# Kernel tuning notes

Measured on AMD Instinct MI355X. Metric: run time of the kernel, lower is better.

Reference implementation:

```python
import jax, jax.numpy as jnp
import numpy as np

LOG_2PI = np.float32(np.log(2.0 * np.pi))


def _expect(features, labels, pi, mu, sigma):
    # features [N,A], labels [N], pi [C,K], mu [C,K,A], sigma [C,K,A,A]
    d = features.shape[1]
    K = pi.shape[1]
    pi_n = pi[labels]                      # [N,K]
    mu_n = mu[labels]                      # [N,K,A]
    # invert / slogdet per (class, cluster) once, then gather (same math as
    # inverting the per-sample gathered sigma, but C*K inversions not N*K)
    inv_sigma = jnp.linalg.inv(sigma)[labels]          # [N,K,A,A]
    logdet = jnp.linalg.slogdet(sigma)[1][labels]      # [N,K]
    diff = features[:, None, :] - mu_n                 # [N,K,A]
    dist = jnp.einsum('nkd,nkde,nke->nk', diff, inv_sigma, diff)
    # NOTE: sign of the d*log(2pi) term follows the original code verbatim
    log_p = -(dist - d * LOG_2PI + logdet) / 2.0       # [N,K]
    onehot = jax.nn.one_hot(jnp.argmax(log_p, axis=1), K, dtype=features.dtype)
    q_un = onehot * pi_n
    return q_un / (q_un.sum(axis=1, keepdims=True) + 1e-30)


def setup_inputs() -> dict:
    key = jax.random.key(0)
    ks = jax.random.split(key, 6)
    N, C, K, A = 2048, 100, 4, 128
    features = jax.random.normal(ks[0], (N, A), dtype=jnp.float32)
    weight = jax.random.normal(ks[1], (C, A), dtype=jnp.float32) * 0.05
    bias = jnp.zeros((C,), dtype=jnp.float32)
    pi = jax.random.uniform(ks[2], (C, K), dtype=jnp.float32) + 0.1
    pi = pi / pi.sum(axis=1, keepdims=True)
    mu = jax.random.normal(ks[3], (C, K, A), dtype=jnp.float32)
    # SPD covariance stack: B B^T / A + I
    B = jax.random.normal(ks[4], (C, K, A, A), dtype=jnp.float32) * 0.3
    sigma = jnp.einsum('ckij,cklj->ckil', B, B) / A + jnp.eye(A, dtype=jnp.float32)
    labels = jax.random.randint(ks[5], (N,), 0, C, dtype=jnp.int64)
    ratio = jnp.float32(0.5)
    return {"features": features, "weight": weight, "bias": bias,
            "pi": pi, "mu": mu, "sigma": sigma, "labels": labels,
            "ratio": ratio}


def reference(features, weight, bias, pi, mu, sigma, labels, ratio):
    N, A = features.shape
    C, K = pi.shape
    y = features @ weight.T + bias                     # fc(features)  [N,C]
    # NxW_ij - NxW_kj : row j of W minus row label[n] of W, per sample
    diff_w = weight[None, :, :] - weight[labels][:, None, :]   # [N,C,A]
    q = _expect(features, labels, pi, mu, sigma)               # [N,K]
    onehot_q = jax.nn.one_hot(jnp.argmax(q, axis=1), K, dtype=features.dtype)
    CV = jnp.einsum('nkde,nk->nde', sigma[labels], onehot_q)   # [N,A,A]
    # diagonal of ratio * (dW) CV (dW)^T, computed without the [N,C,C] matrix
    sigma2 = ratio * jnp.einsum('nca,nab,ncb->nc', diff_w, CV, diff_w)
    aug = y + 0.5 * sigma2                                     # [N,C]
    logp = jax.nn.log_softmax(aug, axis=-1)
    loss = -jnp.mean(jnp.take_along_axis(logp, labels[:, None], axis=1))
    return (loss, y)
```

## Files before the change

kernel.cpp:

```cpp
#include <hip/hip_runtime.h>
#include <hip/hip_bf16.h>
#include <cmath>

#define N_S    2048
#define C_CLS  100
#define K_CL   4
#define A_DIM  128
#define LDSROW 132
#define NB     16
#define MAXPER 96
#define WTPAD  101
#define SPB    8

__global__ __launch_bounds__(256) void k_bucket(
    const int* __restrict__ labels, int* __restrict__ cntg, int* __restrict__ idxg)
{
    __shared__ int cntL[C_CLS];
    const int t = threadIdx.x;
    if (t < C_CLS) cntL[t] = 0;
    __syncthreads();
    for (int n = t; n < N_S; n += 256) {
        int c = labels[n];
        int slot = atomicAdd(&cntL[c], 1);
        if (slot < MAXPER) idxg[c * MAXPER + slot] = n;
    }
    __syncthreads();
    if (t < C_CLS) cntg[t] = min(cntL[t], MAXPER);
}

__device__ __forceinline__ float gj_invert_lds(
    float* As, float* Rbuf, float* DinvS, int tid)
{
    const int lane = tid & 63;
    const int wv   = tid >> 6;
    float logdet = 0.0f;

    for (int t = 0; t < 8; ++t) {
        const int p0 = NB * t;

        if (wv == 0) {
            const int r = lane >> 2, cg = lane & 3;
            float4 dv = *(const float4*)&As[(p0 + r) * LDSROW + p0 + 4 * cg];
            #pragma unroll
            for (int p = 0; p < NB; ++p) {
                const int sel = p & 3, pr4 = p >> 2;
                float te = (sel == 0) ? dv.x : (sel == 1) ? dv.y : (sel == 2) ? dv.z : dv.w;
                float piv = __shfl(te, (p << 2) | pr4, 64);
                float ip  = 1.0f / piv;
                logdet += __logf(piv);
                const int rowsrc = (p << 2) | cg;
                float4 prs;
                prs.x = __shfl(dv.x, rowsrc, 64) * ip;
                prs.y = __shfl(dv.y, rowsrc, 64) * ip;
                prs.z = __shfl(dv.z, rowsrc, 64) * ip;
                prs.w = __shfl(dv.w, rowsrc, 64) * ip;
                if (cg == pr4) (&prs.x)[sel] = ip;
                float f = __shfl(te, (lane & ~3) | pr4, 64);
                if (r == p) {
                    dv = prs;
                } else {
                    dv.x -= f * prs.x; dv.y -= f * prs.y;
                    dv.z -= f * prs.z; dv.w -= f * prs.w;
                    if (cg == pr4) (&dv.x)[sel] = -f * ip;
                }
            }
            DinvS[r * 17 + 4 * cg + 0] = dv.x;
            DinvS[r * 17 + 4 * cg + 1] = dv.y;
            DinvS[r * 17 + 4 * cg + 2] = dv.z;
            DinvS[r * 17 + 4 * cg + 3] = dv.w;
        }
        __syncthreads();

        {
            const int rr = tid >> 5, j4c = tid & 31;
            float4 o;
            if ((j4c >> 2) == t) {
                const int cg = j4c & 3;
                o.x = DinvS[rr * 17 + 4 * cg + 0];
                o.y = DinvS[rr * 17 + 4 * cg + 1];
                o.z = DinvS[rr * 17 + 4 * cg + 2];
                o.w = DinvS[rr * 17 + 4 * cg + 3];
            } else {
                o.x = 0.f; o.y = 0.f; o.z = 0.f; o.w = 0.f;
                #pragma unroll 4
                for (int k = 0; k < NB; ++k) {
                    const float a = DinvS[rr * 17 + k];
                    const float4 s4 = *(const float4*)&As[(p0 + k) * LDSROW + 4 * j4c];
                    o.x += a * s4.x; o.y += a * s4.y; o.z += a * s4.z; o.w += a * s4.w;
                }
            }
            *(float4*)&Rbuf[rr * A_DIM + 4 * j4c] = o;
        }
        __syncthreads();

        if (tid < 448) {
            const int rgi = tid >> 4;
            const int cp  = tid & 15;
            const int rga = (rgi < 4 * t) ? rgi : rgi + 4;
            const int row0 = 4 * rga;
            const int c0 = 8 * cp, c1 = 8 * cp + 4;
            const bool pcol = ((cp >> 1) == t);
            float4 a00, a01, a10, a11, a20, a21, a30, a31;
            if (pcol) {
                a00 = a01 = a10 = a11 = a20 = a21 = a30 = a31 = (float4){0, 0, 0, 0};
            } else {
                a00 = *(const float4*)&As[(row0 + 0) * LDSROW + c0];
                a01 = *(const float4*)&As[(row0 + 0) * LDSROW + c1];
                a10 = *(const float4*)&As[(row0 + 1) * LDSROW + c0];
                a11 = *(const float4*)&As[(row0 + 1) * LDSROW + c1];
                a20 = *(const float4*)&As[(row0 + 2) * LDSROW + c0];
                a21 = *(const float4*)&As[(row0 + 2) * LDSROW + c1];
                a30 = *(const float4*)&As[(row0 + 3) * LDSROW + c0];
                a31 = *(const float4*)&As[(row0 + 3) * LDSROW + c1];
            }
            #pragma unroll 4
            for (int k = 0; k < NB; ++k) {
                const float4 r0 = *(const float4*)&Rbuf[k * A_DIM + c0];
                const float4 r1 = *(const float4*)&Rbuf[k * A_DIM + c1];
                const float f0 = As[(row0 + 0) * LDSROW + p0 + k];
                const float f1 = As[(row0 + 1) * LDSROW + p0 + k];
                const float f2 = As[(row0 + 2) * LDSROW + p0 + k];
                const float f3 = As[(row0 + 3) * LDSROW + p0 + k];
                a00.x -= f0 * r0.x; a00.y -= f0 * r0.y; a00.z -= f0 * r0.z; a00.w -= f0 * r0.w;
                a01.x -= f0 * r1.x; a01.y -= f0 * r1.y; a01.z -= f0 * r1.z; a01.w -= f0 * r1.w;
                a10.x -= f1 * r0.x; a10.y -= f1 * r0.y; a10.z -= f1 * r0.z; a10.w -= f1 * r0.w;
                a11.x -= f1 * r1.x; a11.y -= f1 * r1.y; a11.z -= f1 * r1.z; a11.w -= f1 * r1.w;
                a20.x -= f2 * r0.x; a20.y -= f2 * r0.y; a20.z -= f2 * r0.z; a20.w -= f2 * r0.w;
                a21.x -= f2 * r1.x; a21.y -= f2 * r1.y; a21.z -= f2 * r1.z; a21.w -= f2 * r1.w;
                a30.x -= f3 * r0.x; a30.y -= f3 * r0.y; a30.z -= f3 * r0.z; a30.w -= f3 * r0.w;
                a31.x -= f3 * r1.x; a31.y -= f3 * r1.y; a31.z -= f3 * r1.z; a31.w -= f3 * r1.w;
            }
            *(float4*)&As[(row0 + 0) * LDSROW + c0] = a00;
            *(float4*)&As[(row0 + 0) * LDSROW + c1] = a01;
            *(float4*)&As[(row0 + 1) * LDSROW + c0] = a10;
            *(float4*)&As[(row0 + 1) * LDSROW + c1] = a11;
            *(float4*)&As[(row0 + 2) * LDSROW + c0] = a20;
            *(float4*)&As[(row0 + 2) * LDSROW + c1] = a21;
            *(float4*)&As[(row0 + 3) * LDSROW + c0] = a30;
            *(float4*)&As[(row0 + 3) * LDSROW + c1] = a31;
        }
        {
            const int rr = tid >> 5, j4c = tid & 31;
            *(float4*)&As[(p0 + rr) * LDSROW + 4 * j4c] =
                *(const float4*)&Rbuf[rr * A_DIM + 4 * j4c];
        }
        __syncthreads();
    }
    return logdet;
}

__global__ __launch_bounds__(512, 2) void k_invert_score(
    const float* __restrict__ sigma, const float* __restrict__ mu,
    const float* __restrict__ features, const int* __restrict__ cntg,
    const int* __restrict__ idxg, float* __restrict__ score)
{
    __shared__ __align__(16) float As[A_DIM * LDSROW];
    __shared__ __align__(16) float Scratch[NB * A_DIM + 16*33];
    __shared__ float DinvS[NB * 17];
    __shared__ float ldS;

    const int tid = threadIdx.x;
    const int bid = blockIdx.x;
    const int cl  = bid >> 2;

    const float4* src = (const float4*)(sigma + (size_t)bid * A_DIM * A_DIM);
    for (int e4 = tid; e4 < A_DIM * 32; e4 += 512) {
        int i = e4 >> 5, j4 = e4 & 31;
        *(float4*)&As[i * LDSROW + 4 * j4] = src[e4];
    }
    __syncthreads();

    float logdet = gj_invert_lds(As, Scratch, DinvS, tid);
    if (tid == 0) ldS = logdet;
    __syncthreads();
    const float ld = ldS;

    float* Dbuf = Scratch;
    float* Par  = Scratch + NB * A_DIM;
    const int s16 = tid >> 5;
    const int fc  = tid & 31;
    const int cnt = cntg[cl];
    const float4 muv = ((const float4*)mu)[bid * 32 + fc];

    for (int c0 = 0; c0 < cnt; c0 += 16) {
        const int m = cnt - c0 < 16 ? cnt - c0 : 16;
        if (s16 < m) {
            const int n = idxg[cl * MAXPER + c0 + s16];
            const float4 f = ((const float4*)features)[n * 32 + fc];
            float4 dv;
            dv.x = f.x - muv.x; dv.y = f.y - muv.y;
            dv.z = f.z - muv.z; dv.w = f.w - muv.w;
            *(float4*)&Dbuf[s16 * A_DIM + 4 * fc] = dv;
        }
        __syncthreads();
        if (s16 < m) {
            float4 p = {0.f, 0.f, 0.f, 0.f};
            #pragma unroll 4
            for (int i = 0; i < A_DIM; ++i) {
                const float  d = Dbuf[s16 * A_DIM + i];
                const float4 a = *(const float4*)&As[i * LDSROW + 4 * fc];
                p.x += d * a.x; p.y += d * a.y; p.z += d * a.z; p.w += d * a.w;
            }
            const float4 dj = *(const float4*)&Dbuf[s16 * A_DIM + 4 * fc];
            Par[s16 * 33 + fc] = p.x * dj.x + p.y * dj.y + p.z * dj.z + p.w * dj.w;
        }
        __syncthreads();
        if (tid < m) {
            const int n = idxg[cl * MAXPER + c0 + tid];
            float q = 0.f;
            #pragma unroll
            for (int j = 0; j < 32; ++j) q += Par[tid * 33 + j];
            score[n * K_CL + (bid & 3)] = q + ld;
        }
        __syncthreads();
    }
}

template<int R>
__device__ __forceinline__ void gsweep(
    const float* __restrict__ Ss, const float* __restrict__ weight,
    int c0, int lane, float wc0, float wc1, int bid,
    float* __restrict__ gdiag, float* __restrict__ gcol)
{
    const int c0u = __builtin_amdgcn_readfirstlane(c0);
    const float* __restrict__ wr = weight + (size_t)c0u * A_DIM;
    float h0[R], h1[R];
    #pragma unroll
    for (int r = 0; r < R; ++r) { h0[r] = 0.f; h1[r] = 0.f; }
    #pragma unroll 2
    for (int i = 0; i < A_DIM; ++i) {
        const float s0 = Ss[i * A_DIM + lane];
        const float s1 = Ss[i * A_DIM + 64 + lane];
        #pragma unroll
        for (int r = 0; r < R; ++r) {
            const float b = wr[r * A_DIM + i];
            h0[r] += b * s0; h1[r] += b * s1;
        }
    }
    #pragma unroll
    for (int r = 0; r < R; ++r) {
        const int c = c0 + r;
        float pd = h0[r] * weight[c * A_DIM + lane]
                 + h1[r] * weight[c * A_DIM + 64 + lane];
        float pc = h0[r] * wc0 + h1[r] * wc1;
        #pragma unroll
        for (int off = 32; off; off >>= 1) {
            pd += __shfl_xor(pd, off, 64);
            pc += __shfl_xor(pc, off, 64);
        }
        if (lane == 0) {
            gdiag[bid * C_CLS + c] = pd;
            gcol [bid * C_CLS + c] = pc;
        }
    }
}

__global__ __launch_bounds__(256, 2) void k_gprep(
    const float* __restrict__ sigma, const float* __restrict__ weight,
    float* __restrict__ gdiag, float* __restrict__ gcol)
{
    __shared__ __align__(16) float Ss[A_DIM * A_DIM];
    const int tid = threadIdx.x, bid = blockIdx.x;
    const int cl  = bid >> 2;
    const int lane = tid & 63, wv = tid >> 6;

    const float4* src = (const float4*)(sigma + (size_t)bid * A_DIM * A_DIM);
    for (int e4 = tid; e4 < A_DIM * 32; e4 += 256)
        ((float4*)Ss)[e4] = src[e4];
    __syncthreads();

    const float wc0 = weight[cl * A_DIM + lane];
    const float wc1 = weight[cl * A_DIM + 64 + lane];
    const int cbeg = wv * 25;

    gsweep<10>(Ss, weight, cbeg,      lane, wc0, wc1, bid, gdiag, gcol);
    gsweep<10>(Ss, weight, cbeg + 10, lane, wc0, wc1, bid, gdiag, gcol);
    gsweep<5> (Ss, weight, cbeg + 20, lane, wc0, wc1, bid, gdiag, gcol);
}

__global__ __launch_bounds__(256) void k_out(
    const float* __restrict__ features, const float* __restrict__ weight,
    const float* __restrict__ bias, const int* __restrict__ labels,
    const float* __restrict__ score, const float* __restrict__ gdiag,
    const float* __restrict__ gcol, const float* __restrict__ ratio_p,
    float* __restrict__ y, float* __restrict__ loss)
{
    __shared__ float Wt[A_DIM * WTPAD];
    __shared__ float bs[C_CLS];
    __shared__ __align__(16) float xs[2][A_DIM];
    __shared__ float red[2][2], red2[2][2], acl_s[2], lsum;

    const int tid  = threadIdx.x;
    const int half = tid >> 7;
    const int t    = tid & 127;

    for (int u = tid; u < C_CLS * 32; u += 256) {
        const int c = u >> 5, j4 = u & 31;
        const float4 w = ((const float4*)weight)[u];
        Wt[(4 * j4 + 0) * WTPAD + c] = w.x;
        Wt[(4 * j4 + 1) * WTPAD + c] = w.y;
        Wt[(4 * j4 + 2) * WTPAD + c] = w.z;
        Wt[(4 * j4 + 3) * WTPAD + c] = w.w;
    }
    if (tid < C_CLS) bs[tid] = bias[tid];
    if (tid == 0) lsum = 0.f;
    __syncthreads();

    const float ratio = *ratio_p;

    for (int p = 0; p < SPB; p += 2) {
        const int n = blockIdx.x * SPB + p + half;
        if (t < 32) ((float4*)xs[half])[t] = ((const float4*)features)[n * 32 + t];
        __syncthreads();

        const int cl = labels[n];
        float s0 = score[n * 4 + 0], s1 = score[n * 4 + 1];
        float s2 = score[n * 4 + 2], s3 = score[n * 4 + 3];
        int ks = 0; float bsv = s0;
        if (s1 < bsv) { bsv = s1; ks = 1; }
        if (s2 < bsv) { bsv = s2; ks = 2; }
        if (s3 < bsv) { bsv = s3; ks = 3; }

        const int base = (cl * 4 + ks) * C_CLS;
        const float gll = gdiag[base + cl];
        float aug = -INFINITY;
        if (t < C_CLS) {
            float acc = bs[t];
            #pragma unroll 4
            for (int j = 0; j < A_DIM; ++j)
                acc += xs[half][j] * Wt[j * WTPAD + t];
            y[(size_t)n * C_CLS + t] = acc;
            aug = acc + 0.5f * ratio * (gdiag[base + t] - 2.0f * gcol[base + t] + gll);
        }

        float m = aug;
        #pragma unroll
        for (int off = 32; off; off >>= 1) m = fmaxf(m, __shfl_xor(m, off, 64));
        if ((t & 63) == 0) red[half][t >> 6] = m;
        __syncthreads();
        m = fmaxf(red[half][0], red[half][1]);

        float e = (t < C_CLS) ? expf(aug - m) : 0.0f;
        #pragma unroll
        for (int off = 32; off; off >>= 1) e += __shfl_xor(e, off, 64);
        if ((t & 63) == 0) red2[half][t >> 6] = e;
        if (t == cl) acl_s[half] = aug;
        __syncthreads();

        if (t == 0) {
            float lp = acl_s[half] - m - logf(red2[half][0] + red2[half][1]);
            atomicAdd(&lsum, -lp);
        }
        __syncthreads();
    }
    if (tid == 0) atomicAdd(loss, lsum * (1.0f / (float)N_S));
}

extern "C" void kernel_launch(void* const* d_in, const int* in_sizes, int n_in,
                              void* d_out, int out_size, void* d_ws, size_t ws_size,
                              hipStream_t stream) {
    const float* features = (const float*)d_in[0];
    const float* weight   = (const float*)d_in[1];
    const float* bias     = (const float*)d_in[2];
    const float* mu       = (const float*)d_in[4];
    const float* sigma    = (const float*)d_in[5];
    const int*   labels   = (const int*)d_in[6];
    const float* ratio    = (const float*)d_in[7];

    float* out   = (float*)d_out;
    float* yout  = out + 1;
    float* score = (float*)d_ws;
    float* gdiag = score + N_S * K_CL;
    float* gcol  = gdiag + C_CLS * K_CL * C_CLS;
    int*   cntg  = (int*)(gcol + C_CLS * K_CL * C_CLS);
    int*   idxg  = cntg + C_CLS;

    hipMemsetAsync(d_out, 0, sizeof(float), stream);

    k_bucket      <<<dim3(1),            dim3(256), 0, stream>>>(labels, cntg, idxg);
    k_invert_score<<<dim3(C_CLS * K_CL), dim3(512), 0, stream>>>(sigma, mu, features,
                                                                 cntg, idxg, score);
    k_gprep       <<<dim3(C_CLS * K_CL), dim3(256), 0, stream>>>(sigma, weight, gdiag, gcol);
    k_out         <<<dim3(N_S / SPB),    dim3(256), 0, stream>>>(features, weight, bias, labels,
                                                                 score, gdiag, gcol, ratio, yout, out);
}
```

Baseline: 218.5 us.

## Fuse bucketing, gprep and inversion into one kernel sharing the sigma tile

Removes the single-block bucketing kernel and the separate gprep kernel. Each inversion block now scans the labels itself to collect its class's samples into LDS, and computes the W·Sigma·W products from the sigma tile it has already loaded, before inverting it in place. This saves two kernel launches, a second global read of every sigma matrix, and the serial one-block bucketing step. The cost is extra work per block: the full label scan is repeated in every block, and 8 waves each handle 13 classes with clamping.

```diff
diff --git a/kernel.cpp b/kernel.cpp
--- a/kernel.cpp
+++ b/kernel.cpp
@@ -11,22 +11,6 @@
 #define MAXPER 96
 #define WTPAD  101
 #define SPB    8
-
-__global__ __launch_bounds__(256) void k_bucket(
-    const int* __restrict__ labels, int* __restrict__ cntg, int* __restrict__ idxg)
-{
-    __shared__ int cntL[C_CLS];
-    const int t = threadIdx.x;
-    if (t < C_CLS) cntL[t] = 0;
-    __syncthreads();
-    for (int n = t; n < N_S; n += 256) {
-        int c = labels[n];
-        int slot = atomicAdd(&cntL[c], 1);
-        if (slot < MAXPER) idxg[c * MAXPER + slot] = n;
-    }
-    __syncthreads();
-    if (t < C_CLS) cntg[t] = min(cntL[t], MAXPER);
-}
 
 __device__ __forceinline__ float gj_invert_lds(
     float* As, float* Rbuf, float* DinvS, int tid)
@@ -149,19 +133,72 @@
     return logdet;
 }
 
-__global__ __launch_bounds__(512, 2) void k_invert_score(
+template<int R>
+__device__ __forceinline__ void gsweep(
+    const float* __restrict__ As, const float* __restrict__ weight,
+    int c0, int lane, float wc0, float wc1, int bid,
+    float* __restrict__ gdiag, float* __restrict__ gcol)
+{
+    const int c0u = __builtin_amdgcn_readfirstlane(c0);
+    const float* wr[R];
+    #pragma unroll
+    for (int r = 0; r < R; ++r) {
+        int c = c0u + r; c = (c < C_CLS) ? c : (C_CLS - 1);
+        wr[r] = weight + (size_t)c * A_DIM;
+    }
+    float h0[R], h1[R];
+    #pragma unroll
+    for (int r = 0; r < R; ++r) { h0[r] = 0.f; h1[r] = 0.f; }
+    #pragma unroll 2
+    for (int i = 0; i < A_DIM; ++i) {
+        const float s0 = As[i * LDSROW + lane];
+        const float s1 = As[i * LDSROW + 64 + lane];
+        #pragma unroll
+        for (int r = 0; r < R; ++r) {
+            const float b = wr[r][i];
+            h0[r] += b * s0; h1[r] += b * s1;
+        }
+    }
+    #pragma unroll
+    for (int r = 0; r < R; ++r) {
+        const int c = c0 + r;
+        if (c < C_CLS) {
+            float pd = h0[r] * weight[c * A_DIM + lane]
+                     + h1[r] * weight[c * A_DIM + 64 + lane];
+            float pc = h0[r] * wc0 + h1[r] * wc1;
+            #pragma unroll
+            for (int off = 32; off; off >>= 1) {
+                pd += __shfl_xor(pd, off, 64);
+                pc += __shfl_xor(pc, off, 64);
+            }
+            if (lane == 0) {
+                gdiag[bid * C_CLS + c] = pd;
+                gcol [bid * C_CLS + c] = pc;
+            }
+        }
+    }
+}
+
+__global__ __launch_bounds__(512, 2) void k_fused(
     const float* __restrict__ sigma, const float* __restrict__ mu,
-    const float* __restrict__ features, const int* __restrict__ cntg,
-    const int* __restrict__ idxg, float* __restrict__ score)
+    const float* __restrict__ features, const int* __restrict__ labels,
+    const float* __restrict__ weight, float* __restrict__ score,
+    float* __restrict__ gdiag, float* __restrict__ gcol)
 {
     __shared__ __align__(16) float As[A_DIM * LDSROW];
     __shared__ __align__(16) float Scratch[NB * A_DIM + 16*33];
     __shared__ float DinvS[NB * 17];
     __shared__ float ldS;
-
-    const int tid = threadIdx.x;
-    const int bid = blockIdx.x;
-    const int cl  = bid >> 2;
+    __shared__ int idxL[MAXPER];
+    __shared__ int cntA;
+
+    const int tid  = threadIdx.x;
+    const int bid  = blockIdx.x;
+    const int cl   = bid >> 2;
+    const int lane = tid & 63;
+    const int wv   = tid >> 6;
+
+    if (tid == 0) cntA = 0;
 
     const float4* src = (const float4*)(sigma + (size_t)bid * A_DIM * A_DIM);
     for (int e4 = tid; e4 < A_DIM * 32; e4 += 512) {
@@ -170,22 +207,35 @@
     }
     __syncthreads();
 
+    for (int n = tid; n < N_S; n += 512) {
+        if (labels[n] == cl) {
+            int s = atomicAdd(&cntA, 1);
+            if (s < MAXPER) idxL[s] = n;
+        }
+    }
+    {
+        const float wc0 = weight[cl * A_DIM + lane];
+        const float wc1 = weight[cl * A_DIM + 64 + lane];
+        gsweep<13>(As, weight, wv * 13, lane, wc0, wc1, bid, gdiag, gcol);
+    }
+    __syncthreads();
+
     float logdet = gj_invert_lds(As, Scratch, DinvS, tid);
     if (tid == 0) ldS = logdet;
     __syncthreads();
     const float ld = ldS;
+    const int cnt = min(cntA, MAXPER);
 
     float* Dbuf = Scratch;
     float* Par  = Scratch + NB * A_DIM;
     const int s16 = tid >> 5;
     const int fc  = tid & 31;
-    const int cnt = cntg[cl];
     const float4 muv = ((const float4*)mu)[bid * 32 + fc];
 
     for (int c0 = 0; c0 < cnt; c0 += 16) {
         const int m = cnt - c0 < 16 ? cnt - c0 : 16;
         if (s16 < m) {
-            const int n = idxg[cl * MAXPER + c0 + s16];
+            const int n = idxL[c0 + s16];
             const float4 f = ((const float4*)features)[n * 32 + fc];
             float4 dv;
             dv.x = f.x - muv.x; dv.y = f.y - muv.y;
@@ -206,7 +256,7 @@
         }
         __syncthreads();
         if (tid < m) {
-            const int n = idxg[cl * MAXPER + c0 + tid];
+            const int n = idxL[c0 + tid];
             float q = 0.f;
             #pragma unroll
             for (int j = 0; j < 32; ++j) q += Par[tid * 33 + j];
@@ -214,68 +264,6 @@
         }
         __syncthreads();
     }
-}
-
-template<int R>
-__device__ __forceinline__ void gsweep(
-    const float* __restrict__ Ss, const float* __restrict__ weight,
-    int c0, int lane, float wc0, float wc1, int bid,
-    float* __restrict__ gdiag, float* __restrict__ gcol)
-{
-    const int c0u = __builtin_amdgcn_readfirstlane(c0);
-    const float* __restrict__ wr = weight + (size_t)c0u * A_DIM;
-    float h0[R], h1[R];
-    #pragma unroll
-    for (int r = 0; r < R; ++r) { h0[r] = 0.f; h1[r] = 0.f; }
-    #pragma unroll 2
-    for (int i = 0; i < A_DIM; ++i) {
-        const float s0 = Ss[i * A_DIM + lane];
-        const float s1 = Ss[i * A_DIM + 64 + lane];
-        #pragma unroll
-        for (int r = 0; r < R; ++r) {
-            const float b = wr[r * A_DIM + i];
-            h0[r] += b * s0; h1[r] += b * s1;
-        }
-    }
-    #pragma unroll
-    for (int r = 0; r < R; ++r) {
-        const int c = c0 + r;
-        float pd = h0[r] * weight[c * A_DIM + lane]
-                 + h1[r] * weight[c * A_DIM + 64 + lane];
-        float pc = h0[r] * wc0 + h1[r] * wc1;
-        #pragma unroll
-        for (int off = 32; off; off >>= 1) {
-            pd += __shfl_xor(pd, off, 64);
-            pc += __shfl_xor(pc, off, 64);
-        }
-        if (lane == 0) {
-            gdiag[bid * C_CLS + c] = pd;
-            gcol [bid * C_CLS + c] = pc;
-        }
-    }
-}
-
-__global__ __launch_bounds__(256, 2) void k_gprep(
-    const float* __restrict__ sigma, const float* __restrict__ weight,
-    float* __restrict__ gdiag, float* __restrict__ gcol)
-{
-    __shared__ __align__(16) float Ss[A_DIM * A_DIM];
-    const int tid = threadIdx.x, bid = blockIdx.x;
-    const int cl  = bid >> 2;
-    const int lane = tid & 63, wv = tid >> 6;
-
-    const float4* src = (const float4*)(sigma + (size_t)bid * A_DIM * A_DIM);
-    for (int e4 = tid; e4 < A_DIM * 32; e4 += 256)
-        ((float4*)Ss)[e4] = src[e4];
-    __syncthreads();
-
-    const float wc0 = weight[cl * A_DIM + lane];
-    const float wc1 = weight[cl * A_DIM + 64 + lane];
-    const int cbeg = wv * 25;
-
-    gsweep<10>(Ss, weight, cbeg,      lane, wc0, wc1, bid, gdiag, gcol);
-    gsweep<10>(Ss, weight, cbeg + 10, lane, wc0, wc1, bid, gdiag, gcol);
-    gsweep<5> (Ss, weight, cbeg + 20, lane, wc0, wc1, bid, gdiag, gcol);
 }
 
 __global__ __launch_bounds__(256) void k_out(
@@ -372,15 +360,11 @@
     float* score = (float*)d_ws;
     float* gdiag = score + N_S * K_CL;
     float* gcol  = gdiag + C_CLS * K_CL * C_CLS;
-    int*   cntg  = (int*)(gcol + C_CLS * K_CL * C_CLS);
-    int*   idxg  = cntg + C_CLS;
 
     hipMemsetAsync(d_out, 0, sizeof(float), stream);
 
-    k_bucket      <<<dim3(1),            dim3(256), 0, stream>>>(labels, cntg, idxg);
-    k_invert_score<<<dim3(C_CLS * K_CL), dim3(512), 0, stream>>>(sigma, mu, features,
-                                                                 cntg, idxg, score);
-    k_gprep       <<<dim3(C_CLS * K_CL), dim3(256), 0, stream>>>(sigma, weight, gdiag, gcol);
-    k_out         <<<dim3(N_S / SPB),    dim3(256), 0, stream>>>(features, weight, bias, labels,
-                                                                 score, gdiag, gcol, ratio, yout, out);
-}
+    k_fused<<<dim3(C_CLS * K_CL), dim3(512), 0, stream>>>(sigma, mu, features, labels,
+                                                          weight, score, gdiag, gcol);
+    k_out  <<<dim3(N_S / SPB),    dim3(256), 0, stream>>>(features, weight, bias, labels,
+                                                          score, gdiag, gcol, ratio, yout, out);
+}
```

Measured after the change: 210.5 us. 3.7% less time.
